# Performance work log

Hardware: AMD Instinct MI355X
Metric: run time of the kernel (lower is better)

## Reference

```python
import jax, jax.numpy as jnp
import numpy as np

VIS_DIM, TXT_DIM, HID = 2048, 1024, 1024


def setup_inputs() -> dict:
    key = jax.random.key(0)
    ks = jax.random.split(key, 8)
    def lin(kw, kb, fan_in, fan_out):
        bound = 1.0 / np.sqrt(fan_in)
        W = jax.random.uniform(kw, (fan_out, fan_in), jnp.float32, -bound, bound)
        b = jax.random.uniform(kb, (fan_out,), jnp.float32, -bound, bound)
        return W, b
    Wv, bv = lin(ks[0], ks[1], VIS_DIM, HID)
    Wt, bt = lin(ks[2], ks[3], TXT_DIM, HID)
    Wa, ba = lin(ks[4], ks[5], HID, 1)
    return {
        "visual_features": jax.random.normal(ks[6], (128, 256, VIS_DIM), jnp.float32),
        "text_features": jax.random.normal(ks[7], (128, TXT_DIM), jnp.float32),
        "Wv": Wv, "bv": bv, "Wt": Wt, "bt": bt, "Wa": Wa, "ba": ba,
    }


def reference(visual_features, text_features, Wv, bv, Wt, bt, Wa, ba):
    # v: (B, R, H); t: (B, 1, H) broadcast over regions
    v = jnp.einsum("brd,hd->brh", visual_features, Wv) + bv
    t = (text_features @ Wt.T + bt)[:, None, :]
    combined = jnp.tanh(v + t)                       # (B, R, H)
    scores = jnp.einsum("brh,h->br", combined, Wa[0]) + ba[0]  # (B, R)
    attention_weights = jax.nn.softmax(scores, axis=1)
    attended = jnp.einsum("br,brd->bd", attention_weights, visual_features)
    return attended, attention_weights
```

## Files before the change

kernel.cpp:

```cpp
#include <hip/hip_runtime.h>
#include <hip/hip_bf16.h>

#define VIS_DIM 2048
#define TXT_DIM 1024
#define HID     1024
#define NB      128
#define NR      256
#define M_TOT   (NB*NR)

#define N_ATILES 8192
#define N_TILES  8448
#define TILE_B   16384
#define TSTRIDE  (32 * TILE_B)
#define WS_SCORES_OFF ((size_t)N_TILES * TILE_B)
#define WS_NEED (WS_SCORES_OFF + 131072 + 524288)

typedef __attribute__((ext_vector_type(4))) float  f32x4;
typedef __attribute__((ext_vector_type(8))) short  short8;
typedef __attribute__((ext_vector_type(4))) unsigned short u16x4;

static __device__ __forceinline__ unsigned short f2bf(float f) {
    union { __hip_bfloat16 h; unsigned short u; } c;
    c.h = __float2bfloat16(f);
    return c.u;
}

static __device__ __forceinline__ float bf2f(unsigned short u) {
    union { float f; unsigned u; } c; c.u = ((unsigned)u) << 16; return c.f;
}

static __device__ __forceinline__ float tanh_fast(float x) {
    float xc = fminf(fmaxf(x, -15.f), 15.f);
    float e  = __expf(2.f * xc);
    return (e - 1.f) / (e + 1.f);
}

__global__ __launch_bounds__(256) void prepass(const float* __restrict__ A,
                                               const float* __restrict__ Bv,
                                               unsigned short* __restrict__ w16,
                                               float* __restrict__ scores,
                                               float* __restrict__ tbuf,
                                               const float* __restrict__ bt) {
    const int t   = blockIdx.x;
    const int tid = threadIdx.x;
    if (t < 512) {
        int i = t * 256 + tid;
        if (i < M_TOT) scores[i] = 0.f;
        tbuf[i] = bt[i & (HID - 1)];
    }
    const int mb  = (t < N_ATILES ? t : t - N_ATILES) >> 5;
    const int kt  = t & 31;
    const float* src = (t < N_ATILES ? A : Bv) + (size_t)mb * 128 * VIS_DIM + kt * 64;
    unsigned short* dst = w16 + (size_t)t * (TILE_B / 2);
    #pragma unroll
    for (int i = 0; i < 4; ++i) {
        int si = i * 256 + tid;
        int row = si >> 3, slot = si & 7;
        const float* p = src + (size_t)row * VIS_DIM + slot * 8;
        f32x4 lo = *(const f32x4*)p;
        f32x4 hi = *(const f32x4*)(p + 4);
        short8 v;
        v[0] = (short)f2bf(lo.x); v[1] = (short)f2bf(lo.y);
        v[2] = (short)f2bf(lo.z); v[3] = (short)f2bf(lo.w);
        v[4] = (short)f2bf(hi.x); v[5] = (short)f2bf(hi.y);
        v[6] = (short)f2bf(hi.z); v[7] = (short)f2bf(hi.w);
        *(short8*)(dst + row * 64 + ((slot ^ (row & 7)) << 3)) = v;
    }
}

__global__ void init_ws(float* __restrict__ scores, float* __restrict__ tbuf,
                        const float* __restrict__ bt) {
    int i = blockIdx.x * 256 + threadIdx.x;
    if (i < M_TOT) scores[i] = 0.f;
    tbuf[i] = bt[i & (HID - 1)];
}

__global__ __launch_bounds__(256) void gemm_text(const float* __restrict__ text,
                                                 const float* __restrict__ Wt,
                                                 float* __restrict__ tbuf) {
    __shared__ float As[128][33];
    __shared__ float Bs[32][33];
    const int n0  = blockIdx.x * 32;
    const int k0  = blockIdx.y * 256;
    const int tid = threadIdx.x;
    const int tm  = tid >> 3;
    const int tn  = tid & 7;
    float acc[4][4] = {};
    for (int kt = 0; kt < 8; ++kt) {
        const int k = k0 + kt * 32;
        {
            int row = tid >> 1, off = (tid & 1) * 16;
            const float* src = text + row * TXT_DIM + k + off;
            #pragma unroll
            for (int j = 0; j < 4; ++j) {
                f32x4 v = *(const f32x4*)(src + j * 4);
                As[row][off + j*4 + 0] = v.x; As[row][off + j*4 + 1] = v.y;
                As[row][off + j*4 + 2] = v.z; As[row][off + j*4 + 3] = v.w;
            }
        }
        {
            int row = tid >> 3, off = (tid & 7) * 4;
            f32x4 v = *(const f32x4*)(Wt + (size_t)(n0 + row) * TXT_DIM + k + off);
            Bs[row][off + 0] = v.x; Bs[row][off + 1] = v.y;
            Bs[row][off + 2] = v.z; Bs[row][off + 3] = v.w;
        }
        __syncthreads();
        #pragma unroll
        for (int kk = 0; kk < 32; ++kk) {
            float a[4], b[4];
            #pragma unroll
            for (int i = 0; i < 4; ++i) a[i] = As[tm*4 + i][kk];
            #pragma unroll
            for (int j = 0; j < 4; ++j) b[j] = Bs[tn*4 + j][kk];
            #pragma unroll
            for (int i = 0; i < 4; ++i)
                #pragma unroll
                for (int j = 0; j < 4; ++j) acc[i][j] += a[i] * b[j];
        }
        __syncthreads();
    }
    #pragma unroll
    for (int i = 0; i < 4; ++i)
        #pragma unroll
        for (int j = 0; j < 4; ++j)
            atomicAdd(&tbuf[(tm*4 + i) * HID + n0 + tn*4 + j], acc[i][j]);
}

static __device__ __forceinline__ int toff(int row, int kElem) {
    return row * 128 + ((((kElem >> 3) & 7) ^ (row & 7)) << 4);
}

__global__ __launch_bounds__(512, 2) void gemm_256(
        const unsigned short* __restrict__ w16,
        const float* __restrict__ bv,
        const float* __restrict__ wa,
        const float* __restrict__ tbuf,
        float* __restrict__ scores) {
    __shared__ __align__(16) char lds[131072];

    const int wg   = blockIdx.x;
    const int xcd  = wg & 7;
    const int loc  = wg >> 3;
    const int mb   = xcd * 16 + (loc >> 2);
    const int nb   = loc & 3;
    const int brow = mb * 256;
    const int bcol = nb * 256;

    const int tid  = threadIdx.x;
    const int lane = tid & 63;
    const int wid  = tid >> 6;
    const int wr   = wid >> 2;
    const int wc   = wid & 3;
    const int l    = lane & 15, g = lane >> 4;

    const char* wb = (const char*)w16;
    const char* pA = wb + (size_t)(2 * mb) * TSTRIDE + wid * 1024 + lane * 16;
    const char* pB = wb + (size_t)N_ATILES * TILE_B
                        + (size_t)(2 * nb) * TSTRIDE + wid * 1024 + lane * 16;

    f32x4 acc[8][4] = {};

#define GLOADS(koff, bufbase)                                                  \
    do {                                                                       \
        _Pragma("unroll")                                                      \
        for (int j = 0; j < 8; ++j) {                                          \
            const char* s_ = (j < 4                                            \
                ? pA + (j >> 1) * (size_t)TSTRIDE + (j & 1) * 8192             \
                : pB + ((j - 4) >> 1) * (size_t)TSTRIDE + ((j - 4) & 1) * 8192)\
                + (koff);                                                      \
            __builtin_amdgcn_global_load_lds(                                  \
                (const __attribute__((address_space(1))) float*)s_,            \
                (__attribute__((address_space(3))) float*)                     \
                    (lds + (bufbase) + j * 8192 + wid * 1024),                 \
                16, 0, 0);                                                     \
        }                                                                      \
    } while (0)

#define VWAIT0()                                                               \
    do {                                                                       \
        __builtin_amdgcn_sched_barrier(0);                                     \
        asm volatile("s_waitcnt vmcnt(0)" ::: "memory");                       \
        __builtin_amdgcn_sched_barrier(0);                                     \
    } while (0)

#define BARRIER()                                                              \
    do {                                                                       \
        __builtin_amdgcn_sched_barrier(0);                                     \
        asm volatile("s_waitcnt lgkmcnt(0)" ::: "memory");                     \
        __builtin_amdgcn_s_barrier();                                          \
        __builtin_amdgcn_sched_barrier(0);                                     \
    } while (0)

#define PHASE(bufbase, s)                                                      \
    do {                                                                       \
        const int kE = (s) * 32 + g * 8;                                       \
        const char* pa_ = lds + (bufbase) + wr * 16384;                        \
        const char* pb_ = lds + (bufbase) + 32768 + (wc >> 1) * 16384;         \
        short8 bfr[4], afr[8];                                                 \
        _Pragma("unroll")                                                      \
        for (int n = 0; n < 4; ++n)                                            \
            bfr[n] = *(const short8*)(pb_ + toff((wc & 1) * 64 + n * 16 + l, kE)); \
        _Pragma("unroll")                                                      \
        for (int m = 0; m < 8; ++m)                                            \
            afr[m] = *(const short8*)(pa_ + toff(m * 16 + l, kE));             \
        __builtin_amdgcn_s_setprio(1);                                         \
        _Pragma("unroll")                                                      \
        for (int m = 0; m < 8; ++m) {                                          \
            acc[m][0] = __builtin_amdgcn_mfma_f32_16x16x32_bf16(afr[m], bfr[0], acc[m][0], 0, 0, 0); \
            acc[m][1] = __builtin_amdgcn_mfma_f32_16x16x32_bf16(afr[m], bfr[1], acc[m][1], 0, 0, 0); \
            acc[m][2] = __builtin_amdgcn_mfma_f32_16x16x32_bf16(afr[m], bfr[2], acc[m][2], 0, 0, 0); \
            acc[m][3] = __builtin_amdgcn_mfma_f32_16x16x32_bf16(afr[m], bfr[3], acc[m][3], 0, 0, 0); \
        }                                                                      \
        __builtin_amdgcn_s_setprio(0);                                         \
    } while (0)

    GLOADS((size_t)0, 0);
    VWAIT0();
    GLOADS((size_t)TILE_B, 65536);
    BARRIER();

    #pragma unroll 1
    for (int i = 0; i < 16; ++i) {
        const size_t k2 = (size_t)(2 * i + 2) * TILE_B;
        PHASE(0, 0);
        PHASE(0, 1);
        VWAIT0();
        BARRIER();
        if (i < 15) GLOADS(k2, 0);
        PHASE(65536, 0);
        PHASE(65536, 1);
        if (i < 15) {
            VWAIT0();
            BARRIER();
            GLOADS(k2 + TILE_B, 65536);
        }
    }
#undef GLOADS
#undef VWAIT0
#undef BARRIER
#undef PHASE

    const int b = mb;
    float wa_c[4], bvt_c[4];
    #pragma unroll
    for (int n = 0; n < 4; ++n) {
        int col = bcol + wc * 64 + n * 16 + l;
        wa_c[n]  = wa[col];
        bvt_c[n] = bv[col] + tbuf[b * HID + col];
    }
    #pragma unroll
    for (int m = 0; m < 8; ++m) {
        float p0 = 0.f, p1 = 0.f, p2 = 0.f, p3 = 0.f;
        #pragma unroll
        for (int n = 0; n < 4; ++n) {
            f32x4 v = acc[m][n];
            p0 += wa_c[n] * tanh_fast(v.x + bvt_c[n]);
            p1 += wa_c[n] * tanh_fast(v.y + bvt_c[n]);
            p2 += wa_c[n] * tanh_fast(v.z + bvt_c[n]);
            p3 += wa_c[n] * tanh_fast(v.w + bvt_c[n]);
        }
        #pragma unroll
        for (int d = 1; d < 16; d <<= 1) {
            p0 += __shfl_xor(p0, d); p1 += __shfl_xor(p1, d);
            p2 += __shfl_xor(p2, d); p3 += __shfl_xor(p3, d);
        }
        if ((lane & 15) == 0) {
            int rowg = brow + wr * 128 + m * 16 + g * 4;
            atomicAdd(&scores[rowg + 0], p0);
            atomicAdd(&scores[rowg + 1], p1);
            atomicAdd(&scores[rowg + 2], p2);
            atomicAdd(&scores[rowg + 3], p3);
        }
    }
}

__global__ __launch_bounds__(256) void attend_bf16(
        const unsigned short* __restrict__ w16,
        const float* __restrict__ scores,
        float* __restrict__ out) {
    const int chunk = blockIdx.x;
    const int b     = blockIdx.y;
    const int tid   = threadIdx.x;
    const int lane  = tid & 63;
    const int wv    = tid >> 6;

    __shared__ float wsm[NR];
    __shared__ float red[4];
    __shared__ float part2[4][32][8];

    float s = scores[b * NR + tid];
    float mx = s;
    #pragma unroll
    for (int d = 1; d < 64; d <<= 1) mx = fmaxf(mx, __shfl_xor(mx, d));
    if (lane == 0) red[wv] = mx;
    __syncthreads();
    mx = fmaxf(fmaxf(red[0], red[1]), fmaxf(red[2], red[3]));
    float e = __expf(s - mx);
    float sum = e;
    #pragma unroll
    for (int d = 1; d < 64; d <<= 1) sum += __shfl_xor(sum, d);
    __syncthreads();
    if (lane == 0) red[wv] = sum;
    __syncthreads();
    sum = red[0] + red[1] + red[2] + red[3];
    float w = e * (1.f / sum);
    wsm[tid] = w;
    if (chunk == 0) out[(size_t)NB * VIS_DIM + b * NR + tid] = w;
    __syncthreads();

    const int half  = lane >> 5;
    const int dslot = lane & 31;
    const int d0    = chunk * 256 + dslot * 8;
    const int kt    = d0 >> 6;
    const int ksl   = (d0 >> 3) & 7;
    const int rbase = b * 256 + wv * 64 + half;

    float acc[8] = {};
    #pragma unroll 4
    for (int step = 0; step < 32; ++step) {
        int rowg = rbase + step * 2;
        const char* p = (const char*)w16
            + ((size_t)(rowg >> 7) * 32 + kt) * TILE_B
            + (rowg & 127) * 128 + ((ksl ^ (rowg & 7)) << 4);
        short8 v = *(const short8*)p;
        float w_ = wsm[wv * 64 + step * 2 + half];
        #pragma unroll
        for (int j = 0; j < 8; ++j)
            acc[j] += w_ * bf2f((unsigned short)v[j]);
    }
    #pragma unroll
    for (int j = 0; j < 8; ++j) acc[j] += __shfl_xor(acc[j], 32);

    if (half == 0) {
        #pragma unroll
        for (int j = 0; j < 8; ++j) part2[wv][dslot][j] = acc[j];
    }
    __syncthreads();
    if (wv == 0 && half == 0) {
        float o[8];
        #pragma unroll
        for (int j = 0; j < 8; ++j)
            o[j] = part2[0][dslot][j] + part2[1][dslot][j]
                 + part2[2][dslot][j] + part2[3][dslot][j];
        float* dst = out + (size_t)b * VIS_DIM + chunk * 256 + dslot * 8;
        f32x4 lo = {o[0], o[1], o[2], o[3]};
        f32x4 hi = {o[4], o[5], o[6], o[7]};
        *(f32x4*)dst = lo;
        *(f32x4*)(dst + 4) = hi;
    }
}

#define BK 32
#define NT (VIS_DIM / BK)

static __device__ __forceinline__ int tile_off(int row, int kElem) {
    return row * 64 + (((kElem >> 3) ^ ((row >> 1) & 3)) << 4);
}

__global__ __launch_bounds__(256, 2) void gemm_vis(
        const float* __restrict__ A,
        const float* __restrict__ Bv,
        const float* __restrict__ bv,
        const float* __restrict__ wa,
        const float* __restrict__ tbuf,
        float* __restrict__ scores) {
    __shared__ __align__(16) char lds[32768];

    const int wg   = blockIdx.x;
    const int xcd  = wg & 7;
    const int loc  = wg >> 3;
    const int mb   = xcd * 32 + (loc >> 3);
    const int nb   = loc & 7;
    const int brow = mb * 128;
    const int bcol = nb * 128;

    const int tid  = threadIdx.x;
    const int lane = tid & 63;
    const int wid  = tid >> 6;
    const int wr   = wid >> 1, wc = wid & 1;

    const int srow = tid >> 3;
    const int sfs  = tid & 7;
    unsigned va0 = ((unsigned)(brow + srow      ) * VIS_DIM + sfs * 4) * 4u;
    unsigned va1 = va0 + 32u * VIS_DIM * 4u;
    unsigned va2 = va0 + 64u * VIS_DIM * 4u;
    unsigned va3 = va0 + 96u * VIS_DIM * 4u;
    unsigned vb0 = ((unsigned)(bcol + srow      ) * VIS_DIM + sfs * 4) * 4u;
    unsigned vb1 = vb0 + 32u * VIS_DIM * 4u;
    unsigned vb2 = vb0 + 64u * VIS_DIM * 4u;
    unsigned vb3 = vb0 + 96u * VIS_DIM * 4u;

    int wbyte[4];
    #pragma unroll
    for (int r = 0; r < 4; ++r) {
        int row = srow + 32 * r;
        wbyte[r] = row * 64 + (((sfs >> 1) ^ ((row >> 1) & 3)) << 4) + (sfs & 1) * 8;
    }

    f32x4 sA0, sA1, sA2, sA3, sB0, sB1, sB2, sB3;
    f32x4 tA0, tA1, tA2, tA3, tB0, tB1, tB2, tB3;
    f32x4 acc[4][4] = {};

#define GLOAD_SET(dA0,dA1,dA2,dA3,dB0,dB1,dB2,dB3)                             \
    do {                                                                       \
        asm volatile("global_load_dwordx4 %0, %1, %2"                          \
                     : "=&v"(dA0) : "v"(va0), "s"(A) : "memory");              \
        asm volatile("global_load_dwordx4 %0, %1, %2"                          \
                     : "=&v"(dA1) : "v"(va1), "s"(A) : "memory");              \
        asm volatile("global_load_dwordx4 %0, %1, %2"                          \
                     : "=&v"(dA2) : "v"(va2), "s"(A) : "memory");              \
        asm volatile("global_load_dwordx4 %0, %1, %2"                          \
                     : "=&v"(dA3) : "v"(va3), "s"(A) : "memory");              \
        asm volatile("global_load_dwordx4 %0, %1, %2"                          \
                     : "=&v"(dB0) : "v"(vb0), "s"(Bv) : "memory");             \
        asm volatile("global_load_dwordx4 %0, %1, %2"                          \
                     : "=&v"(dB1) : "v"(vb1), "s"(Bv) : "memory");             \
        asm volatile("global_load_dwordx4 %0, %1, %2"                          \
                     : "=&v"(dB2) : "v"(vb2), "s"(Bv) : "memory");             \
        asm volatile("global_load_dwordx4 %0, %1, %2"                          \
                     : "=&v"(dB3) : "v"(vb3), "s"(Bv) : "memory");             \
        va0 += BK * 4; va1 += BK * 4; va2 += BK * 4; va3 += BK * 4;            \
        vb0 += BK * 4; vb1 += BK * 4; vb2 += BK * 4; vb3 += BK * 4;            \
    } while (0)

#define GLOAD_S() GLOAD_SET(sA0,sA1,sA2,sA3,sB0,sB1,sB2,sB3)
#define GLOAD_T() GLOAD_SET(tA0,tA1,tA2,tA3,tB0,tB1,tB2,tB3)

#define VWAIT(N)                                                               \
    do {                                                                       \
        __builtin_amdgcn_sched_barrier(0);                                     \
        asm volatile("s_waitcnt vmcnt(" #N ")" ::: "memory");                  \
        __builtin_amdgcn_sched_barrier(0);                                     \
    } while (0)

#define BARRIER()                                                              \
    do {                                                                       \
        __builtin_amdgcn_sched_barrier(0);                                     \
        asm volatile("s_waitcnt lgkmcnt(0)" ::: "memory");                     \
        __builtin_amdgcn_s_barrier();                                          \
        __builtin_amdgcn_sched_barrier(0);                                     \
    } while (0)

#define CVT8(dst, v0)                                                          \
    do {                                                                       \
        u16x4 t_;                                                              \
        t_.x = f2bf((v0).x); t_.y = f2bf((v0).y);                              \
        t_.z = f2bf((v0).z); t_.w = f2bf((v0).w);                              \
        dst = t_;                                                              \
    } while (0)

#define LWRITE_SET(bufbase, dA0,dA1,dA2,dA3,dB0,dB1,dB2,dB3)                   \
    do {                                                                       \
        u16x4 w_;                                                              \
        char* la = lds + (bufbase);                                            \
        char* lb = lds + (bufbase) + 8192;                                     \
        CVT8(w_, dA0); *(u16x4*)(la + wbyte[0]) = w_;                          \
        CVT8(w_, dA1); *(u16x4*)(la + wbyte[1]) = w_;                          \
        CVT8(w_, dA2); *(u16x4*)(la + wbyte[2]) = w_;                          \
        CVT8(w_, dA3); *(u16x4*)(la + wbyte[3]) = w_;                          \
        CVT8(w_, dB0); *(u16x4*)(lb + wbyte[0]) = w_;                          \
        CVT8(w_, dB1); *(u16x4*)(lb + wbyte[1]) = w_;                          \
        CVT8(w_, dB2); *(u16x4*)(lb + wbyte[2]) = w_;                          \
        CVT8(w_, dB3); *(u16x4*)(lb + wbyte[3]) = w_;                          \
    } while (0)

#define LWRITE_S(bufbase) LWRITE_SET(bufbase, sA0,sA1,sA2,sA3,sB0,sB1,sB2,sB3)
#define LWRITE_T(bufbase) LWRITE_SET(bufbase, tA0,tA1,tA2,tA3,tB0,tB1,tB2,tB3)

#define COMPUTE(bufbase)                                                       \
    do {                                                                       \
        short8 af[4], bf[4];                                                   \
        const int kk = (lane >> 4) * 8;                                        \
        const char* la = lds + (bufbase);                                      \
        const char* lb = lds + (bufbase) + 8192;                               \
        _Pragma("unroll")                                                      \
        for (int m = 0; m < 4; ++m)                                            \
            af[m] = *(const short8*)(la + tile_off(wr*64 + m*16 + (lane&15), kk)); \
        _Pragma("unroll")                                                      \
        for (int n = 0; n < 4; ++n)                                            \
            bf[n] = *(const short8*)(lb + tile_off(wc*64 + n*16 + (lane&15), kk)); \
        _Pragma("unroll")                                                      \
        for (int m = 0; m < 4; ++m)                                            \
            _Pragma("unroll")                                                  \
            for (int n = 0; n < 4; ++n)                                        \
                acc[m][n] = __builtin_amdgcn_mfma_f32_16x16x32_bf16(           \
                    af[m], bf[n], acc[m][n], 0, 0, 0);                         \
    } while (0)

    GLOAD_S();
    GLOAD_T();
    VWAIT(8);
    LWRITE_S(0);
    BARRIER();

    #pragma unroll 1
    for (int kt = 0; kt < NT - 2; kt += 2) {
        GLOAD_S();
        COMPUTE(0);
        VWAIT(8);
        LWRITE_T(16384);
        BARRIER();
        GLOAD_T();
        COMPUTE(16384);
        VWAIT(8);
        LWRITE_S(0);
        BARRIER();
    }
    COMPUTE(0);
    VWAIT(0);
    LWRITE_T(16384);
    BARRIER();
    COMPUTE(16384);
#undef GLOAD_SET
#undef GLOAD_S
#undef GLOAD_T
#undef VWAIT
#undef BARRIER
#undef CVT8
#undef LWRITE_SET
#undef LWRITE_S
#undef LWRITE_T
#undef COMPUTE

    const int b = brow >> 8;
    float wa_c[4], bvt_c[4];
    #pragma unroll
    for (int n = 0; n < 4; ++n) {
        int col = bcol + wc * 64 + n * 16 + (lane & 15);
        wa_c[n]  = wa[col];
        bvt_c[n] = bv[col] + tbuf[b * HID + col];
    }
    #pragma unroll
    for (int m = 0; m < 4; ++m) {
        float p0 = 0.f, p1 = 0.f, p2 = 0.f, p3 = 0.f;
        #pragma unroll
        for (int n = 0; n < 4; ++n) {
            f32x4 v = acc[m][n];
            p0 += wa_c[n] * tanh_fast(v.x + bvt_c[n]);
            p1 += wa_c[n] * tanh_fast(v.y + bvt_c[n]);
            p2 += wa_c[n] * tanh_fast(v.z + bvt_c[n]);
            p3 += wa_c[n] * tanh_fast(v.w + bvt_c[n]);
        }
        #pragma unroll
        for (int d = 1; d < 16; d <<= 1) {
            p0 += __shfl_xor(p0, d); p1 += __shfl_xor(p1, d);
            p2 += __shfl_xor(p2, d); p3 += __shfl_xor(p3, d);
        }
        if ((lane & 15) == 0) {
            int rowg = brow + wr * 64 + m * 16 + (lane >> 4) * 4;
            atomicAdd(&scores[rowg + 0], p0);
            atomicAdd(&scores[rowg + 1], p1);
            atomicAdd(&scores[rowg + 2], p2);
            atomicAdd(&scores[rowg + 3], p3);
        }
    }
}

__global__ __launch_bounds__(256) void attend(const float* __restrict__ visual,
                                              const float* __restrict__ scores,
                                              float* __restrict__ out) {
    const int chunk = blockIdx.x;
    const int b     = blockIdx.y;
    const int tid   = threadIdx.x;
    const int lane  = tid & 63;
    const int wv    = tid >> 6;

    __shared__ float wsm[NR];
    __shared__ float red[4];
    __shared__ f32x4 part[4][64];

    float s = scores[b * NR + tid];
    float mx = s;
    #pragma unroll
    for (int d = 1; d < 64; d <<= 1) mx = fmaxf(mx, __shfl_xor(mx, d));
    if (lane == 0) red[wv] = mx;
    __syncthreads();
    mx = fmaxf(fmaxf(red[0], red[1]), fmaxf(red[2], red[3]));
    float e = __expf(s - mx);
    float sum = e;
    #pragma unroll
    for (int d = 1; d < 64; d <<= 1) sum += __shfl_xor(sum, d);
    __syncthreads();
    if (lane == 0) red[wv] = sum;
    __syncthreads();
    sum = red[0] + red[1] + red[2] + red[3];
    float w = e * (1.f / sum);
    wsm[tid] = w;
    if (chunk == 0) out[(size_t)NB * VIS_DIM + b * NR + tid] = w;
    __syncthreads();

    const float* vb = visual + ((size_t)b * NR + wv * 64) * VIS_DIM + chunk * 256 + lane * 4;
    f32x4 acc = {0.f, 0.f, 0.f, 0.f};
    #pragma unroll
    for (int r = 0; r < 64; r += 4) {
        f32x4 v0 = *(const f32x4*)(vb + (size_t)(r + 0) * VIS_DIM);
        f32x4 v1 = *(const f32x4*)(vb + (size_t)(r + 1) * VIS_DIM);
        f32x4 v2 = *(const f32x4*)(vb + (size_t)(r + 2) * VIS_DIM);
        f32x4 v3 = *(const f32x4*)(vb + (size_t)(r + 3) * VIS_DIM);
        acc += wsm[wv * 64 + r + 0] * v0;
        acc += wsm[wv * 64 + r + 1] * v1;
        acc += wsm[wv * 64 + r + 2] * v2;
        acc += wsm[wv * 64 + r + 3] * v3;
    }
    part[wv][lane] = acc;
    __syncthreads();
    if (wv == 0) {
        f32x4 a = part[0][lane] + part[1][lane] + part[2][lane] + part[3][lane];
        *(f32x4*)(out + (size_t)b * VIS_DIM + chunk * 256 + lane * 4) = a;
    }
}

extern "C" void kernel_launch(void* const* d_in, const int* in_sizes, int n_in,
                              void* d_out, int out_size, void* d_ws, size_t ws_size,
                              hipStream_t stream) {
    (void)in_sizes; (void)n_in; (void)out_size;
    const float* visual = (const float*)d_in[0];
    const float* text   = (const float*)d_in[1];
    const float* Wv     = (const float*)d_in[2];
    const float* bv     = (const float*)d_in[3];
    const float* Wt     = (const float*)d_in[4];
    const float* bt     = (const float*)d_in[5];
    const float* Wa     = (const float*)d_in[6];

    float* out = (float*)d_out;
    const bool fast = ws_size >= (size_t)WS_NEED;

    if (fast) {
        unsigned short* w16 = (unsigned short*)d_ws;
        float* scores = (float*)((char*)d_ws + WS_SCORES_OFF);
        float* tbuf   = scores + M_TOT;
        prepass    <<<N_TILES, 256, 0, stream>>>(visual, Wv, w16, scores, tbuf, bt);
        gemm_text  <<<dim3(32, 4), 256, 0, stream>>>(text, Wt, tbuf);
        gemm_256   <<<512, 512, 0, stream>>>(w16, bv, Wa, tbuf, scores);
        attend_bf16<<<dim3(8, NB), 256, 0, stream>>>(w16, scores, out);
    } else {
        float* scores = (float*)d_ws;
        float* tbuf   = scores + M_TOT;
        init_ws  <<<512, 256, 0, stream>>>(scores, tbuf, bt);
        gemm_text<<<dim3(32, 4), 256, 0, stream>>>(text, Wt, tbuf);
        gemm_vis <<<2048, 256, 0, stream>>>(visual, Wv, bv, Wa, tbuf, scores);
        attend   <<<dim3(8, NB), 256, 0, stream>>>(visual, scores, out);
    }
}
```

Before: 245.9 us.

## Use 4 waves with 128x128 warp tiles in the bf16 attention GEMM

```diff
diff --git a/kernel.cpp b/kernel.cpp
--- a/kernel.cpp
+++ b/kernel.cpp
@@ -130,7 +130,7 @@
     return row * 128 + ((((kElem >> 3) & 7) ^ (row & 7)) << 4);
 }
 
-__global__ __launch_bounds__(512, 2) void gemm_256(
+__global__ __launch_bounds__(256, 1) void gemm_256(
         const unsigned short* __restrict__ w16,
         const float* __restrict__ bv,
         const float* __restrict__ wa,
@@ -149,29 +149,28 @@
     const int tid  = threadIdx.x;
     const int lane = tid & 63;
     const int wid  = tid >> 6;
-    const int wr   = wid >> 2;
-    const int wc   = wid & 3;
+    const int wr   = wid >> 1;
+    const int wc   = wid & 1;
     const int l    = lane & 15, g = lane >> 4;
 
     const char* wb = (const char*)w16;
-    const char* pA = wb + (size_t)(2 * mb) * TSTRIDE + wid * 1024 + lane * 16;
-    const char* pB = wb + (size_t)N_ATILES * TILE_B
-                        + (size_t)(2 * nb) * TSTRIDE + wid * 1024 + lane * 16;
-
-    f32x4 acc[8][4] = {};
+    const char* pW = (wid < 2)
+        ? wb + (size_t)(2 * mb + wid) * TSTRIDE + lane * 16
+        : wb + (size_t)N_ATILES * TILE_B
+             + (size_t)(2 * nb + (wid - 2)) * TSTRIDE + lane * 16;
+    const int ldsW = wid * 16384;
+
+    f32x4 acc[8][8] = {};
 
 #define GLOADS(koff, bufbase)                                                  \
     do {                                                                       \
         _Pragma("unroll")                                                      \
-        for (int j = 0; j < 8; ++j) {                                          \
-            const char* s_ = (j < 4                                            \
-                ? pA + (j >> 1) * (size_t)TSTRIDE + (j & 1) * 8192             \
-                : pB + ((j - 4) >> 1) * (size_t)TSTRIDE + ((j - 4) & 1) * 8192)\
-                + (koff);                                                      \
+        for (int j = 0; j < 16; ++j) {                                         \
             __builtin_amdgcn_global_load_lds(                                  \
-                (const __attribute__((address_space(1))) float*)s_,            \
+                (const __attribute__((address_space(1))) float*)               \
+                    (pW + (koff) + j * 1024),                                  \
                 (__attribute__((address_space(3))) float*)                     \
-                    (lds + (bufbase) + j * 8192 + wid * 1024),                 \
+                    (lds + (bufbase) + ldsW + j * 1024),                       \
                 16, 0, 0);                                                     \
         }                                                                      \
     } while (0)
@@ -195,22 +194,21 @@
     do {                                                                       \
         const int kE = (s) * 32 + g * 8;                                       \
         const char* pa_ = lds + (bufbase) + wr * 16384;                        \
-        const char* pb_ = lds + (bufbase) + 32768 + (wc >> 1) * 16384;         \
-        short8 bfr[4], afr[8];                                                 \
+        const char* pb_ = lds + (bufbase) + 32768 + wc * 16384;                \
+        short8 bfr[8], afr[8];                                                 \
         _Pragma("unroll")                                                      \
-        for (int n = 0; n < 4; ++n)                                            \
-            bfr[n] = *(const short8*)(pb_ + toff((wc & 1) * 64 + n * 16 + l, kE)); \
+        for (int n = 0; n < 8; ++n)                                            \
+            bfr[n] = *(const short8*)(pb_ + toff(n * 16 + l, kE));             \
         _Pragma("unroll")                                                      \
         for (int m = 0; m < 8; ++m)                                            \
             afr[m] = *(const short8*)(pa_ + toff(m * 16 + l, kE));             \
         __builtin_amdgcn_s_setprio(1);                                         \
         _Pragma("unroll")                                                      \
-        for (int m = 0; m < 8; ++m) {                                          \
-            acc[m][0] = __builtin_amdgcn_mfma_f32_16x16x32_bf16(afr[m], bfr[0], acc[m][0], 0, 0, 0); \
-            acc[m][1] = __builtin_amdgcn_mfma_f32_16x16x32_bf16(afr[m], bfr[1], acc[m][1], 0, 0, 0); \
-            acc[m][2] = __builtin_amdgcn_mfma_f32_16x16x32_bf16(afr[m], bfr[2], acc[m][2], 0, 0, 0); \
-            acc[m][3] = __builtin_amdgcn_mfma_f32_16x16x32_bf16(afr[m], bfr[3], acc[m][3], 0, 0, 0); \
-        }                                                                      \
+        for (int m = 0; m < 8; ++m)                                            \
+            _Pragma("unroll")                                                  \
+            for (int n = 0; n < 8; ++n)                                        \
+                acc[m][n] = __builtin_amdgcn_mfma_f32_16x16x32_bf16(           \
+                    afr[m], bfr[n], acc[m][n], 0, 0, 0);                       \
         __builtin_amdgcn_s_setprio(0);                                         \
     } while (0)
 
@@ -241,10 +239,10 @@
 #undef PHASE
 
     const int b = mb;
-    float wa_c[4], bvt_c[4];
-    #pragma unroll
-    for (int n = 0; n < 4; ++n) {
-        int col = bcol + wc * 64 + n * 16 + l;
+    float wa_c[8], bvt_c[8];
+    #pragma unroll
+    for (int n = 0; n < 8; ++n) {
+        int col = bcol + wc * 128 + n * 16 + l;
         wa_c[n]  = wa[col];
         bvt_c[n] = bv[col] + tbuf[b * HID + col];
     }
@@ -252,7 +250,7 @@
     for (int m = 0; m < 8; ++m) {
         float p0 = 0.f, p1 = 0.f, p2 = 0.f, p3 = 0.f;
         #pragma unroll
-        for (int n = 0; n < 4; ++n) {
+        for (int n = 0; n < 8; ++n) {
             f32x4 v = acc[m][n];
             p0 += wa_c[n] * tanh_fast(v.x + bvt_c[n]);
             p1 += wa_c[n] * tanh_fast(v.y + bvt_c[n]);
@@ -631,7 +629,7 @@
         float* tbuf   = scores + M_TOT;
         prepass    <<<N_TILES, 256, 0, stream>>>(visual, Wv, w16, scores, tbuf, bt);
         gemm_text  <<<dim3(32, 4), 256, 0, stream>>>(text, Wt, tbuf);
-        gemm_256   <<<512, 512, 0, stream>>>(w16, bv, Wa, tbuf, scores);
+        gemm_256   <<<512, 256, 0, stream>>>(w16, bv, Wa, tbuf, scores);
         attend_bf16<<<dim3(8, NB), 256, 0, stream>>>(w16, scores, out);
     } else {
         float* scores = (float*)d_ws;
```

Result: slower. 314.7 us (+28.0%).
